# Kernel optimization log

Measured on AMD Instinct MI355X. Metric: run time of the kernel, lower is better.

The kernel has to match this reference:

```python
import jax, jax.numpy as jnp
import numpy as np

B, L, N = 4, 1024, 2048
V_DIM, L_DIM, HID, H = 512, 768, 512, 8
HD = HID // H
SCALE = HD ** -0.5


def setup_inputs() -> dict:
    key = jax.random.key(0)
    ks = jax.random.split(key, 6)
    return {
        "x": jax.random.normal(ks[0], (B, L, V_DIM), dtype=jnp.float32),
        "vfeats": jax.random.normal(ks[1], (B, N, L_DIM), dtype=jnp.float32),
        "topk_mask": jax.random.normal(ks[2], (B, H, L, N), dtype=jnp.float32),
        "Wq": jax.random.normal(ks[3], (HID, V_DIM), dtype=jnp.float32) * 0.02,
        "Wkv": jax.random.normal(ks[4], (2 * HID, L_DIM), dtype=jnp.float32) * 0.02,
        "Wproj": jax.random.normal(ks[5], (V_DIM, HID), dtype=jnp.float32) * 0.02,
        "bproj": jnp.zeros((V_DIM,), dtype=jnp.float32),
    }


def reference(x, vfeats, topk_mask, Wq, Wkv, Wproj, bproj):
    # q: [B,L,HID] -> [B,H,L,HD]
    q = (x @ Wq.T).reshape(B, L, H, HD).transpose(0, 2, 1, 3)
    # kv: [B,N,2*HID] -> k,v each [B,H,N,HD]
    kv = (vfeats @ Wkv.T).reshape(B, N, 2, H, HD).transpose(2, 0, 3, 1, 4)
    k, v = kv[0], kv[1]
    attn = jnp.einsum("bhld,bhnd->bhln", q, k) * SCALE + topk_mask
    attn = jax.nn.softmax(attn, axis=-1)
    out = jnp.einsum("bhln,bhnd->bhld", attn, v)  # [B,H,L,HD]
    out = out.transpose(0, 2, 1, 3).reshape(B, L, HID)
    return out @ Wproj.T + bproj
```

## Files before the change

kernel.cpp:

```cpp
#include <hip/hip_runtime.h>
#include <math.h>

#define B_ 4
#define L_ 1024
#define N_ 2048
#define VDIM_ 512
#define LDIM_ 768
#define HID_ 512
#define H_ 8
#define HD_ 64
#define SCALE_ 0.125f

typedef __bf16 bf16;
typedef __bf16 bf16x4 __attribute__((ext_vector_type(4)));
typedef __bf16 bf16x8 __attribute__((ext_vector_type(8)));
typedef float f32x4 __attribute__((ext_vector_type(4)));

__device__ __forceinline__ void async_cp16(const bf16* g, bf16* l) {
    __builtin_amdgcn_global_load_lds(
        (const __attribute__((address_space(1))) unsigned int*)g,
        (__attribute__((address_space(3))) unsigned int*)l, 16, 0, 0);
}

#define XE_   2097152
#define VFE_  6291456
#define WQE_  262144
#define WKVE_ 786432
#define WPE_  262144
__global__ void cvt_all(const float* __restrict__ x, const float* __restrict__ vf,
                        const float* __restrict__ wq, const float* __restrict__ wkv,
                        const float* __restrict__ wp,
                        bf16* __restrict__ xb, bf16* __restrict__ vfb,
                        bf16* __restrict__ wqb, bf16* __restrict__ wkvb,
                        bf16* __restrict__ wph, bf16* __restrict__ wpl)
{
    int e = (blockIdx.x * 256 + threadIdx.x) * 4;
    if (e < XE_ + VFE_ + WQE_ + WKVE_) {
        const float* src; bf16* dst; int off;
        if (e < XE_)                        { src = x;   dst = xb;   off = 0; }
        else if (e < XE_ + VFE_)            { src = vf;  dst = vfb;  off = XE_; }
        else if (e < XE_ + VFE_ + WQE_)     { src = wq;  dst = wqb;  off = XE_ + VFE_; }
        else                                { src = wkv; dst = wkvb; off = XE_ + VFE_ + WQE_; }
        int i = e - off;
        float4 v = *(const float4*)(src + i);
        bf16x4 o;
        o[0] = (bf16)v.x; o[1] = (bf16)v.y; o[2] = (bf16)v.z; o[3] = (bf16)v.w;
        *(bf16x4*)(dst + i) = o;
    } else {
        int i = e - (XE_ + VFE_ + WQE_ + WKVE_);
        float4 v = *(const float4*)(wp + i);
        bf16x4 hh, ll;
        float vv[4] = {v.x, v.y, v.z, v.w};
        #pragma unroll
        for (int j = 0; j < 4; ++j) {
            bf16 hb = (bf16)vv[j];
            hh[j] = hb;
            ll[j] = (bf16)(vv[j] - (float)hb);
        }
        *(bf16x4*)(wph + i) = hh;
        *(bf16x4*)(wpl + i) = ll;
    }
}

template<int BM, int BN>
__global__ __launch_bounds__(256)
void gemm_bf16(const bf16* __restrict__ A, const bf16* __restrict__ W,
               bf16* __restrict__ C, int M, int N, int K)
{
    __shared__ bf16 As[BM * 64];
    __shared__ bf16 Ws[BN * 64];
    const int t = threadIdx.x, l = t & 63, wv = t >> 6;
    const int n0 = blockIdx.x * BN, m0 = blockIdx.y * BM;
    const int wm = (wv >> 1) * (BM / 2), wn = (wv & 1) * (BN / 2);
    constexpr int TI = BM / 32, TJ = BN / 32;
    const int lq = l & 15, qd = l >> 4, swz = l & 7;

    f32x4 acc[TI][TJ];
    #pragma unroll
    for (int i = 0; i < TI; ++i)
        #pragma unroll
        for (int j = 0; j < TJ; ++j)
            #pragma unroll
            for (int r = 0; r < 4; ++r) acc[i][j][r] = 0.f;

    for (int kt = 0; kt < K; kt += 64) {
        __syncthreads();
        for (int it = wv; it < BM / 8; it += 4) {
            int r = it * 8 + (l >> 3);
            int c = (l & 7) ^ (r & 7);
            async_cp16(A + (size_t)(m0 + r) * K + kt + c * 8, &As[it * 512]);
        }
        for (int it = wv; it < BN / 8; it += 4) {
            int r = it * 8 + (l >> 3);
            int c = (l & 7) ^ (r & 7);
            async_cp16(W + (size_t)(n0 + r) * K + kt + c * 8, &Ws[it * 512]);
        }
        __syncthreads();
        #pragma unroll
        for (int ks = 0; ks < 2; ++ks) {
            bf16x8 af[TI], wf[TJ];
            #pragma unroll
            for (int i = 0; i < TI; ++i) {
                int row = wm + i * 16 + lq;
                af[i] = *(const bf16x8*)&As[row * 64 + ((ks * 4 + qd) ^ swz) * 8];
            }
            #pragma unroll
            for (int j = 0; j < TJ; ++j) {
                int row = wn + j * 16 + lq;
                wf[j] = *(const bf16x8*)&Ws[row * 64 + ((ks * 4 + qd) ^ swz) * 8];
            }
            #pragma unroll
            for (int i = 0; i < TI; ++i)
                #pragma unroll
                for (int j = 0; j < TJ; ++j)
                    acc[i][j] = __builtin_amdgcn_mfma_f32_16x16x32_bf16(
                        af[i], wf[j], acc[i][j], 0, 0, 0);
        }
    }
    #pragma unroll
    for (int i = 0; i < TI; ++i)
        #pragma unroll
        for (int j = 0; j < TJ; ++j)
            #pragma unroll
            for (int r = 0; r < 4; ++r) {
                int row = m0 + wm + i * 16 + qd * 4 + r;
                int col = n0 + wn + j * 16 + lq;
                C[(size_t)row * N + col] = (bf16)acc[i][j][r];
            }
}

__global__ __launch_bounds__(256)
void gemm_proj(const bf16* __restrict__ A, const bf16* __restrict__ Wh,
               const bf16* __restrict__ Wl, const float* __restrict__ bias,
               float* __restrict__ Cf, int M, int N, int K)
{
    __shared__ bf16 sA[64 * 64];
    __shared__ bf16 sWh[64 * 64], sWl[64 * 64];
    const int t = threadIdx.x, l = t & 63, wv = t >> 6;
    const int n0 = blockIdx.x * 64, m0 = blockIdx.y * 64;
    const int wm = (wv >> 1) * 32, wn = (wv & 1) * 32;
    const int lq = l & 15, qd = l >> 4, swz = l & 7;

    f32x4 acc[2][2];
    #pragma unroll
    for (int i = 0; i < 2; ++i)
        #pragma unroll
        for (int j = 0; j < 2; ++j)
            #pragma unroll
            for (int r = 0; r < 4; ++r) acc[i][j][r] = 0.f;

    for (int kt = 0; kt < K; kt += 64) {
        __syncthreads();
        for (int it = wv; it < 8; it += 4) {
            int r = it * 8 + (l >> 3);
            int c = (l & 7) ^ (r & 7);
            async_cp16(A  + (size_t)(m0 + r) * K + kt + c * 8, &sA[it * 512]);
            size_t go = (size_t)(n0 + r) * K + kt + c * 8;
            async_cp16(Wh + go, &sWh[it * 512]);
            async_cp16(Wl + go, &sWl[it * 512]);
        }
        __syncthreads();
        #pragma unroll
        for (int ks = 0; ks < 2; ++ks) {
            bf16x8 af[2], wh[2], wl[2];
            #pragma unroll
            for (int i = 0; i < 2; ++i) {
                int off = (wm + i * 16 + lq) * 64 + ((ks * 4 + qd) ^ swz) * 8;
                af[i] = *(const bf16x8*)&sA[off];
            }
            #pragma unroll
            for (int j = 0; j < 2; ++j) {
                int off = (wn + j * 16 + lq) * 64 + ((ks * 4 + qd) ^ swz) * 8;
                wh[j] = *(const bf16x8*)&sWh[off];
                wl[j] = *(const bf16x8*)&sWl[off];
            }
            #pragma unroll
            for (int i = 0; i < 2; ++i)
                #pragma unroll
                for (int j = 0; j < 2; ++j) {
                    acc[i][j] = __builtin_amdgcn_mfma_f32_16x16x32_bf16(af[i], wh[j], acc[i][j], 0, 0, 0);
                    acc[i][j] = __builtin_amdgcn_mfma_f32_16x16x32_bf16(af[i], wl[j], acc[i][j], 0, 0, 0);
                }
        }
    }
    #pragma unroll
    for (int i = 0; i < 2; ++i)
        #pragma unroll
        for (int j = 0; j < 2; ++j) {
            int col = n0 + wn + j * 16 + lq;
            float bb = bias[col];
            #pragma unroll
            for (int r = 0; r < 4; ++r) {
                int row = m0 + wm + i * 16 + qd * 4 + r;
                Cf[(size_t)row * N + col] = acc[i][j][r] + bb;
            }
        }
}

__global__ __launch_bounds__(256)
void transpose_v(const bf16* __restrict__ kv, bf16* __restrict__ vT)
{
    __shared__ bf16 T[64 * 64];
    const int t = threadIdx.x;
    const int bid = blockIdx.x;
    const int nt = bid & 31, h = (bid >> 5) & 7, b = bid >> 8;
    const int n0 = nt * 64;
    for (int g = t; g < 512; g += 256) {
        int r = g >> 3, c = g & 7;
        bf16x8 v = *(const bf16x8*)(kv + (size_t)(b * N_ + n0 + r) * (2 * HID_) +
                                    HID_ + h * HD_ + c * 8);
        *(bf16x8*)&T[r * 64 + (c ^ (r & 7)) * 8] = v;
    }
    __syncthreads();
    for (int g = t; g < 512; g += 256) {
        int d = g >> 3, kg = g & 7;
        bf16x8 ov;
        #pragma unroll
        for (int jj = 0; jj < 8; ++jj) {
            int key = kg * 8 + jj;
            ov[jj] = T[key * 64 + (((d >> 3) ^ (key & 7))) * 8 + (d & 7)];
        }
        *(bf16x8*)&vT[(size_t)((b * H_ + h) * HD_ + d) * N_ + n0 + kg * 8] = ov;
    }
}

#define KT_ 64
#define NT_ 32
#define PST 72
__global__ __launch_bounds__(256)
void attn_mfma(const bf16* __restrict__ q, const bf16* __restrict__ kv,
               const bf16* __restrict__ vT, const float* __restrict__ mask,
               bf16* __restrict__ ao)
{
    __shared__ bf16 Ks[2][64 * 64];
    __shared__ bf16 Vs[2][64 * 64];
    __shared__ bf16 Pa[4][16 * PST];
    const int t = threadIdx.x, l = t & 63, wv = t >> 6;
    const int bid0 = blockIdx.x;
    const int bid = (bid0 & 7) * 64 + (bid0 >> 3);
    const int lt = bid & 15, h = (bid >> 4) & 7, b = bid >> 7;
    const int l0 = lt * 64;
    const int lq = l & 15, qd = l >> 4, swz = l & 7;
    const int sr = l >> 3;
    const int sc8 = ((l & 7) ^ sr) * 8;

    bf16x8 qf[2];
    {
        const bf16* qb = q + (size_t)(b * L_ + l0 + wv * 16 + lq) * HID_ + h * HD_ + qd * 8;
        qf[0] = *(const bf16x8*)qb;
        qf[1] = *(const bf16x8*)(qb + 32);
    }

    f32x4 o[4];
    #pragma unroll
    for (int j = 0; j < 4; ++j)
        #pragma unroll
        for (int r = 0; r < 4; ++r) o[j][r] = 0.f;
    float m_run[4], l_run[4];
    #pragma unroll
    for (int r = 0; r < 4; ++r) { m_run[r] = -1e30f; l_run[r] = 0.f; }

    const bf16* kb = kv + (size_t)(b * N_) * (2 * HID_) + h * HD_;
    const bf16* vb = vT + (size_t)((b * H_ + h) * HD_) * N_;
    const size_t mrow0 = (size_t)((b * H_ + h) * L_ + l0 + wv * 16);
    bf16* Paw = &Pa[wv][0];

    float mkA[4][4], mkB[4][4];

#define STAGE(BUF, NTILE) do {                                                  \
    const int nb_ = (NTILE) * KT_;                                              \
    _Pragma("unroll")                                                           \
    for (int it_ = 0; it_ < 2; ++it_) {                                         \
        int r_ = (wv + it_ * 4) * 8 + sr;                                       \
        async_cp16(kb + (size_t)(nb_ + r_) * (2 * HID_) + sc8,                  \
                   &Ks[BUF][(wv + it_ * 4) * 512]);                             \
    }                                                                           \
    _Pragma("unroll")                                                           \
    for (int it_ = 0; it_ < 2; ++it_) {                                         \
        int r_ = (wv + it_ * 4) * 8 + sr;                                       \
        async_cp16(vb + (size_t)r_ * N_ + nb_ + sc8,                            \
                   &Vs[BUF][(wv + it_ * 4) * 512]);                             \
    }                                                                           \
} while (0)

#define MASKLOAD(DST, NTILE) do {                                               \
    const int nb_ = (NTILE) * KT_;                                              \
    _Pragma("unroll")                                                           \
    for (int jj = 0; jj < 4; ++jj)                                              \
        _Pragma("unroll")                                                       \
        for (int r = 0; r < 4; ++r)                                             \
            DST[jj][r] = mask[(mrow0 + qd * 4 + r) * N_ + nb_ + jj * 16 + lq];  \
} while (0)

#define ATTN_ITER(NTI, CB, NB, MKC, MKN) do {                                   \
    if ((NTI) + 1 < NT_) {                                                      \
        STAGE(NB, (NTI) + 1);                                                   \
        __builtin_amdgcn_sched_barrier(0);                                      \
        MASKLOAD(MKN, (NTI) + 1);                                               \
        __builtin_amdgcn_sched_barrier(0);                                      \
    }                                                                           \
                                              \
    f32x4 s[4];                                                                 \
    _Pragma("unroll")                                                           \
    for (int jj = 0; jj < 4; ++jj)                                              \
        _Pragma("unroll")                                                       \
        for (int r = 0; r < 4; ++r) s[jj][r] = 0.f;                             \
    _Pragma("unroll")                                                           \
    for (int ks = 0; ks < 2; ++ks)                                              \
        _Pragma("unroll")                                                       \
        for (int jj = 0; jj < 4; ++jj) {                                        \
            bf16x8 kf = *(const bf16x8*)&Ks[CB][(jj * 16 + lq) * 64 +           \
                                               ((ks * 4 + qd) ^ swz) * 8];      \
            s[jj] = __builtin_amdgcn_mfma_f32_16x16x32_bf16(qf[ks], kf, s[jj], 0, 0, 0); \
        }                                                                       \
    _Pragma("unroll")                                                           \
    for (int jj = 0; jj < 4; ++jj)                                              \
        _Pragma("unroll")                                                       \
        for (int r = 0; r < 4; ++r)                                             \
            s[jj][r] = fmaf(s[jj][r], SCALE_, MKC[jj][r]);                      \
            \
    float alpha[4], mnew[4];                                                    \
    _Pragma("unroll")                                                           \
    for (int r = 0; r < 4; ++r) {                                               \
        float mx = fmaxf(fmaxf(s[0][r], s[1][r]), fmaxf(s[2][r], s[3][r]));     \
        _Pragma("unroll")                                                       \
        for (int d2 = 1; d2 < 16; d2 <<= 1) mx = fmaxf(mx, __shfl_xor(mx, d2)); \
        mnew[r] = fmaxf(m_run[r], mx);                                          \
        alpha[r] = __expf(m_run[r] - mnew[r]);                                  \
        m_run[r] = mnew[r];                                                     \
    }                                                                           \
    _Pragma("unroll")                                                           \
    for (int r = 0; r < 4; ++r) {                                               \
        float ss = 0.f;                                                         \
        _Pragma("unroll")                                                       \
        for (int jj = 0; jj < 4; ++jj) {                                        \
            float p = __expf(s[jj][r] - mnew[r]);                               \
            Paw[(qd * 4 + r) * PST + jj * 16 + lq] = (bf16)p;                   \
            ss += p;                                                            \
        }                                                                       \
        _Pragma("unroll")                                                       \
        for (int d2 = 1; d2 < 16; d2 <<= 1) ss += __shfl_xor(ss, d2);           \
        l_run[r] = l_run[r] * alpha[r] + ss;                                    \
    }                                                                           \
    asm volatile("s_waitcnt lgkmcnt(0)" ::: "memory");                          \
    __builtin_amdgcn_sched_barrier(0);                                          \
                                      \
    _Pragma("unroll")                                                           \
    for (int jj = 0; jj < 4; ++jj)                                              \
        _Pragma("unroll")                                                       \
        for (int r = 0; r < 4; ++r) o[jj][r] *= alpha[r];                       \
    _Pragma("unroll")                                                           \
    for (int ks = 0; ks < 2; ++ks) {                                            \
        bf16x8 pf = *(const bf16x8*)&Paw[lq * PST + ks * 32 + qd * 8];          \
        _Pragma("unroll")                                                       \
        for (int jj = 0; jj < 4; ++jj) {                                        \
            bf16x8 vf = *(const bf16x8*)&Vs[CB][(jj * 16 + lq) * 64 +           \
                                               ((ks * 4 + qd) ^ swz) * 8];      \
            o[jj] = __builtin_amdgcn_mfma_f32_16x16x32_bf16(pf, vf, o[jj], 0, 0, 0); \
        }                                                                       \
    }                                                                           \
     \
    __builtin_amdgcn_sched_barrier(0);                                          \
    asm volatile("s_waitcnt vmcnt(16)" ::: "memory");                           \
    __builtin_amdgcn_s_barrier();                                               \
    __builtin_amdgcn_sched_barrier(0);                                          \
} while (0)

    STAGE(0, 0);
    MASKLOAD(mkA, 0);
    __syncthreads();

    #pragma unroll 1
    for (int nt2 = 0; nt2 < NT_; nt2 += 2) {
        ATTN_ITER(nt2,     0, 1, mkA, mkB);
        ATTN_ITER(nt2 + 1, 1, 0, mkB, mkA);
    }
#undef ATTN_ITER
#undef MASKLOAD
#undef STAGE

    #pragma unroll
    for (int jj = 0; jj < 4; ++jj)
        #pragma unroll
        for (int r = 0; r < 4; ++r) {
            int row = b * L_ + l0 + wv * 16 + qd * 4 + r;
            int col = h * HD_ + jj * 16 + lq;
            ao[(size_t)row * HID_ + col] = (bf16)(o[jj][r] / l_run[r]);
        }
}

extern "C" void kernel_launch(void* const* d_in, const int* in_sizes, int n_in,
                              void* d_out, int out_size, void* d_ws, size_t ws_size,
                              hipStream_t stream)
{
    const float* x      = (const float*)d_in[0];
    const float* vfeats = (const float*)d_in[1];
    const float* mask   = (const float*)d_in[2];
    const float* Wq     = (const float*)d_in[3];
    const float* Wkv    = (const float*)d_in[4];
    const float* Wproj  = (const float*)d_in[5];
    const float* bproj  = (const float*)d_in[6];
    float* out = (float*)d_out;

    char* ws = (char*)d_ws;
    bf16* xb   = (bf16*)(ws);
    bf16* vfb  = (bf16*)(ws + 4194304);
    bf16* wqb  = (bf16*)(ws + 16777216);
    bf16* wkvb = (bf16*)(ws + 17301504);
    bf16* wph  = (bf16*)(ws + 18874368);
    bf16* wpl  = (bf16*)(ws + 19398656);
    bf16* qb   = (bf16*)(ws + 19922944);
    bf16* kvb  = (bf16*)(ws + 24117248);
    bf16* vTb  = (bf16*)(ws + 40894464);
    bf16* aob  = (bf16*)(ws + 49283072);

    dim3 blk(256);
    cvt_all<<<dim3((XE_ + VFE_ + WQE_ + WKVE_ + WPE_) / 1024), blk, 0, stream>>>(
        x, vfeats, Wq, Wkv, Wproj, xb, vfb, wqb, wkvb, wph, wpl);
    gemm_bf16<64, 64><<<dim3(HID_ / 64, B_ * L_ / 64), blk, 0, stream>>>(
        xb, wqb, qb, B_ * L_, HID_, VDIM_);
    gemm_bf16<128, 128><<<dim3(2 * HID_ / 128, B_ * N_ / 128), blk, 0, stream>>>(
        vfb, wkvb, kvb, B_ * N_, 2 * HID_, LDIM_);
    transpose_v<<<dim3(B_ * H_ * (N_ / 64)), blk, 0, stream>>>(kvb, vTb);
    attn_mfma<<<dim3(B_ * H_ * (L_ / 64)), blk, 0, stream>>>(qb, kvb, vTb, mask, aob);
    gemm_proj<<<dim3(VDIM_ / 64, B_ * L_ / 64), blk, 0, stream>>>(
        aob, wph, wpl, bproj, out, B_ * L_, VDIM_, HID_);
}
```

Measured before the change: 452.8 us.

## Fuse Q and KV projections with V transpose into one launch

Merges the Q projection GEMM, the KV projection GEMM and the separate V transpose kernel into one grouped kernel of 1536 blocks. V-half tiles are transposed through shared memory in the epilogue and written straight into the vT layout, so the V half of kv is never written and reread. The KV GEMM tile changes from 128x128 to 128x64. Mask loads in attention now use nontemporal loads to avoid polluting cache. This saves launches and a memory round trip but mixes heterogeneous block shapes in one grid.

After: 446.9 us. Within noise of the previous version (-1.3%).

```diff
diff --git a/kernel.cpp b/kernel.cpp
--- a/kernel.cpp
+++ b/kernel.cpp
@@ -63,19 +63,16 @@
 }
 
 template<int BM, int BN>
-__global__ __launch_bounds__(256)
-void gemm_bf16(const bf16* __restrict__ A, const bf16* __restrict__ W,
-               bf16* __restrict__ C, int M, int N, int K)
-{
-    __shared__ bf16 As[BM * 64];
-    __shared__ bf16 Ws[BN * 64];
-    const int t = threadIdx.x, l = t & 63, wv = t >> 6;
-    const int n0 = blockIdx.x * BN, m0 = blockIdx.y * BM;
-    const int wm = (wv >> 1) * (BM / 2), wn = (wv & 1) * (BN / 2);
+__device__ __forceinline__ void gemm_core(
+    const bf16* __restrict__ A, const bf16* __restrict__ W,
+    bf16* __restrict__ As, bf16* __restrict__ Ws,
+    int m0, int n0, int K, int l, int wv,
+    f32x4 (&acc)[BM / 32][BN / 32])
+{
     constexpr int TI = BM / 32, TJ = BN / 32;
     const int lq = l & 15, qd = l >> 4, swz = l & 7;
-
-    f32x4 acc[TI][TJ];
+    const int wm = (wv >> 1) * (BM / 2), wn = (wv & 1) * (BN / 2);
+
     #pragma unroll
     for (int i = 0; i < TI; ++i)
         #pragma unroll
@@ -117,16 +114,81 @@
                         af[i], wf[j], acc[i][j], 0, 0, 0);
         }
     }
-    #pragma unroll
-    for (int i = 0; i < TI; ++i)
-        #pragma unroll
-        for (int j = 0; j < TJ; ++j)
-            #pragma unroll
-            for (int r = 0; r < 4; ++r) {
-                int row = m0 + wm + i * 16 + qd * 4 + r;
-                int col = n0 + wn + j * 16 + lq;
-                C[(size_t)row * N + col] = (bf16)acc[i][j][r];
-            }
+}
+
+#define TST 136
+__global__ __launch_bounds__(256)
+void gemm_qkv(const bf16* __restrict__ xb, const bf16* __restrict__ wqb,
+              bf16* __restrict__ qb,
+              const bf16* __restrict__ vfb, const bf16* __restrict__ wkvb,
+              bf16* __restrict__ kvb, bf16* __restrict__ vTb)
+{
+    __shared__ bf16 pool[128 * 64 + 64 * 64];
+    bf16* As = pool;
+    bf16* Ws = pool + 128 * 64;
+    const int t = threadIdx.x, l = t & 63, wv = t >> 6;
+    const int lq = l & 15, qd = l >> 4;
+    const int o = blockIdx.x;
+    const int bid = (o & 7) * 192 + (o >> 3);
+
+    if (bid < 512) {
+        const int n0 = (bid & 7) * 64, m0 = (bid >> 3) * 64;
+        f32x4 acc[2][2];
+        gemm_core<64, 64>(xb, wqb, As, Ws, m0, n0, VDIM_, l, wv, acc);
+        const int wm = (wv >> 1) * 32, wn = (wv & 1) * 32;
+        #pragma unroll
+        for (int i = 0; i < 2; ++i)
+            #pragma unroll
+            for (int j = 0; j < 2; ++j)
+                #pragma unroll
+                for (int r = 0; r < 4; ++r) {
+                    int row = m0 + wm + i * 16 + qd * 4 + r;
+                    int col = n0 + wn + j * 16 + lq;
+                    qb[(size_t)row * HID_ + col] = (bf16)acc[i][j][r];
+                }
+    } else {
+        const int v = bid - 512;
+        const int n0 = (v & 15) * 64, m0 = (v >> 4) * 128;
+        f32x4 acc[4][2];
+        gemm_core<128, 64>(vfb, wkvb, As, Ws, m0, n0, LDIM_, l, wv, acc);
+        const int wm = (wv >> 1) * 64, wn = (wv & 1) * 32;
+        if (n0 < HID_) {
+            #pragma unroll
+            for (int i = 0; i < 4; ++i)
+                #pragma unroll
+                for (int j = 0; j < 2; ++j)
+                    #pragma unroll
+                    for (int r = 0; r < 4; ++r) {
+                        int row = m0 + wm + i * 16 + qd * 4 + r;
+                        int col = n0 + wn + j * 16 + lq;
+                        kvb[(size_t)row * (2 * HID_) + col] = (bf16)acc[i][j][r];
+                    }
+        } else {
+            __syncthreads();
+            bf16* T = pool;
+            #pragma unroll
+            for (int i = 0; i < 4; ++i)
+                #pragma unroll
+                for (int j = 0; j < 2; ++j)
+                    #pragma unroll
+                    for (int r = 0; r < 4; ++r) {
+                        int nl = wm + i * 16 + qd * 4 + r;
+                        int dl = wn + j * 16 + lq;
+                        T[dl * TST + nl] = (bf16)acc[i][j][r];
+                    }
+            __syncthreads();
+            const int b = m0 >> 11, h = (n0 - HID_) >> 6;
+            const int nrow0 = m0 & (N_ - 1);
+            bf16* dst = vTb + (size_t)((b * H_ + h) * HD_) * N_ + nrow0;
+            #pragma unroll
+            for (int rep = 0; rep < 4; ++rep) {
+                int id = rep * 256 + t;
+                int d = id >> 4, c = id & 15;
+                bf16x8 val = *(const bf16x8*)&T[d * TST + c * 8];
+                *(bf16x8*)&dst[(size_t)d * N_ + c * 8] = val;
+            }
+        }
+    }
 }
 
 __global__ __launch_bounds__(256)
@@ -195,33 +257,6 @@
                 Cf[(size_t)row * N + col] = acc[i][j][r] + bb;
             }
         }
-}
-
-__global__ __launch_bounds__(256)
-void transpose_v(const bf16* __restrict__ kv, bf16* __restrict__ vT)
-{
-    __shared__ bf16 T[64 * 64];
-    const int t = threadIdx.x;
-    const int bid = blockIdx.x;
-    const int nt = bid & 31, h = (bid >> 5) & 7, b = bid >> 8;
-    const int n0 = nt * 64;
-    for (int g = t; g < 512; g += 256) {
-        int r = g >> 3, c = g & 7;
-        bf16x8 v = *(const bf16x8*)(kv + (size_t)(b * N_ + n0 + r) * (2 * HID_) +
-                                    HID_ + h * HD_ + c * 8);
-        *(bf16x8*)&T[r * 64 + (c ^ (r & 7)) * 8] = v;
-    }
-    __syncthreads();
-    for (int g = t; g < 512; g += 256) {
-        int d = g >> 3, kg = g & 7;
-        bf16x8 ov;
-        #pragma unroll
-        for (int jj = 0; jj < 8; ++jj) {
-            int key = kg * 8 + jj;
-            ov[jj] = T[key * 64 + (((d >> 3) ^ (key & 7))) * 8 + (d & 7)];
-        }
-        *(bf16x8*)&vT[(size_t)((b * H_ + h) * HD_ + d) * N_ + n0 + kg * 8] = ov;
-    }
 }
 
 #define KT_ 64
@@ -289,7 +324,8 @@
     for (int jj = 0; jj < 4; ++jj)                                              \
         _Pragma("unroll")                                                       \
         for (int r = 0; r < 4; ++r)                                             \
-            DST[jj][r] = mask[(mrow0 + qd * 4 + r) * N_ + nb_ + jj * 16 + lq];  \
+            DST[jj][r] = __builtin_nontemporal_load(                            \
+                mask + (mrow0 + qd * 4 + r) * N_ + nb_ + jj * 16 + lq);         \
 } while (0)
 
 #define ATTN_ITER(NTI, CB, NB, MKC, MKN) do {                                   \
@@ -417,11 +453,7 @@
     dim3 blk(256);
     cvt_all<<<dim3((XE_ + VFE_ + WQE_ + WKVE_ + WPE_) / 1024), blk, 0, stream>>>(
         x, vfeats, Wq, Wkv, Wproj, xb, vfb, wqb, wkvb, wph, wpl);
-    gemm_bf16<64, 64><<<dim3(HID_ / 64, B_ * L_ / 64), blk, 0, stream>>>(
-        xb, wqb, qb, B_ * L_, HID_, VDIM_);
-    gemm_bf16<128, 128><<<dim3(2 * HID_ / 128, B_ * N_ / 128), blk, 0, stream>>>(
-        vfb, wkvb, kvb, B_ * N_, 2 * HID_, LDIM_);
-    transpose_v<<<dim3(B_ * H_ * (N_ / 64)), blk, 0, stream>>>(kvb, vTb);
+    gemm_qkv<<<dim3(1536), blk, 0, stream>>>(xb, wqb, qb, vfb, wkvb, kvb, vTb);
     attn_mfma<<<dim3(B_ * H_ * (L_ / 64)), blk, 0, stream>>>(qb, kvb, vTb, mask, aob);
     gemm_proj<<<dim3(VDIM_ / 64, B_ * L_ / 64), blk, 0, stream>>>(
         aob, wph, wpl, bproj, out, B_ * L_, VDIM_, HID_);
```
